# Kernel tuning notes

Hardware: AMD Instinct MI355X
Metric: run time of the kernel (lower is better)

Reference implementation:

```python
import jax, jax.numpy as jnp
import numpy as np


def setup_inputs() -> dict:
    key = jax.random.key(0)
    k1, k2 = jax.random.split(key)
    N, D, O, K = 65536, 256, 256, 8  # tokens, inputdim, outdim, degree+1
    gridsize = 8
    x = jax.random.normal(k1, (N, D), dtype=jnp.float32)
    # init stddev = 1/(sqrt(inputdim)*sqrt(gridsize)) as in the module
    std = 1.0 / (np.sqrt(D) * np.sqrt(gridsize))
    cheby_coeffs = jax.random.normal(k2, (O, D, K), dtype=jnp.float32) * std
    bias = jnp.zeros((1, O), dtype=jnp.float32)
    return {"x": x, "cheby_coeffs": cheby_coeffs, "bias": bias}


def reference(x, cheby_coeffs, bias):
    # x: (N, D); cheby_coeffs: (O, D, K); bias: (1, O)
    K = cheby_coeffs.shape[-1]
    xt = jnp.tanh(x)                       # squash into [-1, 1]
    theta = jnp.arccos(xt)                 # (N, D)
    n = jnp.arange(K, dtype=x.dtype)       # Chebyshev orders 0..degree
    # T_n(xt) = cos(n * arccos(xt)), matching the original per-degree loop
    T = jnp.cos(theta[..., None] * n)      # (N, D, K)
    y = jnp.einsum('ndk,odk->no', T, cheby_coeffs)  # (N, O)
    y = y + bias
    return y
```

## Files before the change

kernel.cpp:

```cpp
#include <hip/hip_runtime.h>
#include <hip/hip_bf16.h>

typedef __attribute__((ext_vector_type(4)))  int   i32x4;
typedef __attribute__((ext_vector_type(16))) int   i32x16;

#define DIM_D 256
#define DIM_O 256
#define DIM_K 8
#define BM 128
#define NCHUNK 16
#define NSTEP 4
#define MAGIC 12582912.f

__global__ __launch_bounds__(256) void pack_w_kernel(
    const float* __restrict__ coeffs,
    unsigned int* __restrict__ wp,
    float* __restrict__ scales)
{
    const int o = blockIdx.x;
    const int d = threadIdx.x;
    const float* cp = coeffs + ((size_t)o * DIM_D + d) * DIM_K;
    float4 c0 = *(const float4*)cp;
    float4 c1 = *(const float4*)(cp + 4);

    float m = fmaxf(fmaxf(fmaxf(fabsf(c0.x), fabsf(c0.y)),
                          fmaxf(fabsf(c0.z), fabsf(c0.w))),
                    fmaxf(fmaxf(fabsf(c1.x), fabsf(c1.y)),
                          fmaxf(fabsf(c1.z), fabsf(c1.w))));
    #pragma unroll
    for (int i = 32; i >= 1; i >>= 1)
        m = fmaxf(m, __shfl_xor(m, i));
    __shared__ float wm[4];
    if ((d & 63) == 0) wm[d >> 6] = m;
    __syncthreads();
    const float sc = fmaxf(fmaxf(fmaxf(wm[0], wm[1]), fmaxf(wm[2], wm[3])),
                           1e-30f);
    if (d == 0) scales[o] = sc;

    const float inv = 127.0f / sc;
    unsigned f0 = __float_as_uint(__builtin_fmaf(c0.x, inv, MAGIC));
    unsigned f1 = __float_as_uint(__builtin_fmaf(c0.y, inv, MAGIC));
    unsigned f2 = __float_as_uint(__builtin_fmaf(c0.z, inv, MAGIC));
    unsigned f3 = __float_as_uint(__builtin_fmaf(c0.w, inv, MAGIC));
    unsigned f4 = __float_as_uint(__builtin_fmaf(c1.x, inv, MAGIC));
    unsigned f5 = __float_as_uint(__builtin_fmaf(c1.y, inv, MAGIC));
    unsigned f6 = __float_as_uint(__builtin_fmaf(c1.z, inv, MAGIC));
    unsigned f7 = __float_as_uint(__builtin_fmaf(c1.w, inv, MAGIC));
    unsigned rA = __builtin_amdgcn_perm(f1, f0, 0x00000400u);
    unsigned rB = __builtin_amdgcn_perm(f3, f2, 0x00000400u);
    unsigned rC = __builtin_amdgcn_perm(f5, f4, 0x00000400u);
    unsigned rD = __builtin_amdgcn_perm(f7, f6, 0x00000400u);
    unsigned lo = __builtin_amdgcn_perm(rB, rA, 0x05040100u);
    unsigned hi = __builtin_amdgcn_perm(rD, rC, 0x05040100u);

    const int base = (((d >> 2) * 8 + (o >> 5)) * 64
                      + ((d >> 1) & 1) * 32 + (o & 31)) * 4 + (d & 1) * 2;
    wp[base]     = lo;
    wp[base + 1] = hi;
}

__device__ __forceinline__ void cheb_q8(float xs, unsigned int* o2) {
    float e2 = __expf(2.f * xs);
    float r  = __builtin_amdgcn_rcpf(e2 + 1.f);
    float T1 = __builtin_fmaf(-2.f, r, 1.f);
    float tx = T1 + T1;
    float T2 = __builtin_fmaf(tx, T1, -1.f);
    float T3 = __builtin_fmaf(tx, T2, -T1);
    float T4 = __builtin_fmaf(tx, T3, -T2);
    float T5 = __builtin_fmaf(tx, T4, -T3);
    float T6 = __builtin_fmaf(tx, T5, -T4);
    float T7 = __builtin_fmaf(tx, T6, -T5);
    unsigned f1 = __float_as_uint(__builtin_fmaf(T1, 127.f, MAGIC));
    unsigned f2 = __float_as_uint(__builtin_fmaf(T2, 127.f, MAGIC));
    unsigned f3 = __float_as_uint(__builtin_fmaf(T3, 127.f, MAGIC));
    unsigned f4 = __float_as_uint(__builtin_fmaf(T4, 127.f, MAGIC));
    unsigned f5 = __float_as_uint(__builtin_fmaf(T5, 127.f, MAGIC));
    unsigned f6 = __float_as_uint(__builtin_fmaf(T6, 127.f, MAGIC));
    unsigned f7 = __float_as_uint(__builtin_fmaf(T7, 127.f, MAGIC));
    unsigned rA = __builtin_amdgcn_perm(f2, f1, 0x00000400u);
    unsigned rC = __builtin_amdgcn_perm(f5, f4, 0x00000400u);
    unsigned rD = __builtin_amdgcn_perm(f7, f6, 0x00000400u);
    o2[0] = __builtin_amdgcn_perm(f3, rA, 0x0401000Cu) | 127u;
    o2[1] = __builtin_amdgcn_perm(rD, rC, 0x05040100u);
}

__global__ __launch_bounds__(256, 2) void cfkan_kernel(
    const float* __restrict__ x,
    const i32x4* __restrict__ wp8,
    const float* __restrict__ scales,
    const float* __restrict__ bias,
    float* __restrict__ y)
{
    __shared__ unsigned char Abuf[2][BM][128];

    const int t = threadIdx.x;
    const int w = t >> 6;
    const int l = t & 63;
    const int m = l & 31;
    const int h = l >> 5;
    const int bid = (int)blockIdx.x;
    const int cpx = (int)gridDim.x >> 3;
    const int row0 = ((bid & 7) * cpx + (bid >> 3)) * BM;

    i32x16 acc[4][2];
    #pragma unroll
    for (int rt = 0; rt < 4; ++rt)
        #pragma unroll
        for (int ct = 0; ct < 2; ++ct)
            #pragma unroll
            for (int qi = 0; qi < 16; ++qi)
                acc[rt][ct][qi] = 0;

    const int lrow = t >> 1;
    const int half = t & 1;
    const float* xrow = x + (size_t)(row0 + lrow) * DIM_D + half * 8;

#define READA(DST, AB, S) do {                                             \
    const int _so = (((2 * (S) + h) ^ (m & 7)) * 16);                      \
    DST[0] = *(const i32x4*)&AB[      m][_so];                             \
    DST[1] = *(const i32x4*)&AB[ 32 + m][_so];                             \
    DST[2] = *(const i32x4*)&AB[ 64 + m][_so];                             \
    DST[3] = *(const i32x4*)&AB[ 96 + m][_so];                             \
} while (0)
#define LOADB2(DST, SG) do {                                               \
    DST[0] = wp8[((SG) * 8 + w * 2 + 0) * 64 + l];                         \
    DST[1] = wp8[((SG) * 8 + w * 2 + 1) * 64 + l];                         \
} while (0)
#define STAGE2(ANX, S, X0, X1) do {                                        \
    union { unsigned int u[4]; i32x4 v; } _tv;                             \
    cheb_q8(X0, &_tv.u[0]);                                                \
    cheb_q8(X1, &_tv.u[2]);                                                \
    *(i32x4*)&ANX[lrow][(((half * 4 + (S)) ^ (lrow & 7)) * 16)] = _tv.v;   \
} while (0)
#define SOFT_BARRIER() do {                                                \
    asm volatile("s_waitcnt lgkmcnt(0)" ::: "memory");                     \
    __builtin_amdgcn_s_barrier();                                          \
    __builtin_amdgcn_sched_barrier(0);                                     \
} while (0)

    float xv[8];
    {
        float4 a0 = *(const float4*)xrow;
        float4 a1 = *(const float4*)(xrow + 4);
        float xs[8] = {a0.x, a0.y, a0.z, a0.w, a1.x, a1.y, a1.z, a1.w};
        #pragma unroll
        for (int s = 0; s < 4; ++s)
            STAGE2(Abuf[0], s, xs[2 * s], xs[2 * s + 1]);
        float4 b0 = *(const float4*)(xrow + 16);
        float4 b1 = *(const float4*)(xrow + 16 + 4);
        xv[0] = b0.x; xv[1] = b0.y; xv[2] = b0.z; xv[3] = b0.w;
        xv[4] = b1.x; xv[5] = b1.y; xv[6] = b1.z; xv[7] = b1.w;
    }
    i32x4 bq[NSTEP + 2][2];
    LOADB2(bq[0], 0);
    LOADB2(bq[1], 1);
    SOFT_BARRIER();
    i32x4 r[4], rn[4];
    READA(r, Abuf[0], 0);

    #pragma unroll 1
    for (int c = 0; c < NCHUNK; ++c) {
        const unsigned char (*A)[128] = Abuf[c & 1];
        unsigned char (*ANX)[128]     = Abuf[(c & 1) ^ 1];
        const bool stage = (c < NCHUNK - 1);
        float4 xn0, xn1;
        if (c + 2 < NCHUNK) {
            xn0 = *(const float4*)(xrow + (c + 2) * 16);
            xn1 = *(const float4*)(xrow + (c + 2) * 16 + 4);
        }

        #pragma unroll
        for (int s = 0; s < NSTEP; ++s) {
            LOADB2(bq[s + 2], (c * 4 + s + 2) & 63);
            if (s < NSTEP - 1) READA(rn, A, s + 1);

            __builtin_amdgcn_s_setprio(1);
            #pragma unroll
            for (int rt = 0; rt < 4; ++rt) {
                acc[rt][0] = __builtin_amdgcn_mfma_i32_32x32x32_i8(
                    r[rt], bq[s][0], acc[rt][0], 0, 0, 0);
                acc[rt][1] = __builtin_amdgcn_mfma_i32_32x32x32_i8(
                    r[rt], bq[s][1], acc[rt][1], 0, 0, 0);
            }
            __builtin_amdgcn_s_setprio(0);

            if (stage) STAGE2(ANX, s, xv[2 * s], xv[2 * s + 1]);

            if (s < NSTEP - 1) { r[0] = rn[0]; r[1] = rn[1]; r[2] = rn[2]; r[3] = rn[3]; }
        }
        bq[0][0] = bq[4][0]; bq[0][1] = bq[4][1];
        bq[1][0] = bq[5][0]; bq[1][1] = bq[5][1];
        if (c + 2 < NCHUNK) {
            xv[0] = xn0.x; xv[1] = xn0.y; xv[2] = xn0.z; xv[3] = xn0.w;
            xv[4] = xn1.x; xv[5] = xn1.y; xv[6] = xn1.z; xv[7] = xn1.w;
        }
        SOFT_BARRIER();
        if (c < NCHUNK - 1) READA(r, ANX, 0);
    }

    #pragma unroll
    for (int ct = 0; ct < 2; ++ct) {
        const int col = w * 64 + ct * 32 + m;
        const float sf = scales[col] * (1.f / 16129.f);
        const float bv = bias[col];
        #pragma unroll
        for (int rt = 0; rt < 4; ++rt) {
            #pragma unroll
            for (int qi = 0; qi < 16; ++qi) {
                const int grow = row0 + rt * 32 + (qi & 3) + 8 * (qi >> 2) + 4 * h;
                y[(size_t)grow * DIM_O + col] =
                    __builtin_fmaf((float)acc[rt][ct][qi], sf, bv);
            }
        }
    }
#undef READA
#undef LOADB2
#undef STAGE2
#undef SOFT_BARRIER
}

extern "C" void kernel_launch(void* const* d_in, const int* in_sizes, int n_in,
                              void* d_out, int out_size, void* d_ws, size_t ws_size,
                              hipStream_t stream) {
    const float* x      = (const float*)d_in[0];
    const float* coeffs = (const float*)d_in[1];
    const float* bias   = (const float*)d_in[2];
    float* y = (float*)d_out;
    float*        scales = (float*)d_ws;
    unsigned int* wp     = (unsigned int*)((char*)d_ws + 1024);

    const int n_tokens = in_sizes[0] / DIM_D;

    pack_w_kernel<<<DIM_O, 256, 0, stream>>>(coeffs, wp, scales);
    cfkan_kernel<<<n_tokens / BM, 256, 0, stream>>>(
        x, (const i32x4*)wp, scales, bias, y);
}
```

Measured before the change: 54.32 us.

## Double K-chunk size to halve barriers and restage A in second half

Each chunk now covers 32 input features instead of 16, so the LDS A-buffer doubles to 256 bytes per row and the main loop runs 8 iterations with 8 MFMA steps each, halving the number of block barriers. The x prefetch distance drops from two chunks to one. The Chebyshev quantize-and-store of the next chunk is moved into steps 4-7 of the current chunk. The B register ring grows to 10 entries, which raises VGPR pressure, and the shorter x prefetch distance may expose global load latency. LDS per block doubles as well, so occupancy at 2 blocks per CU may be at risk.

```diff
diff --git a/kernel.cpp b/kernel.cpp
--- a/kernel.cpp
+++ b/kernel.cpp
@@ -8,8 +8,8 @@
 #define DIM_O 256
 #define DIM_K 8
 #define BM 128
-#define NCHUNK 16
-#define NSTEP 4
+#define NCHUNK 8
+#define NSTEP 8
 #define MAGIC 12582912.f
 
 __global__ __launch_bounds__(256) void pack_w_kernel(
@@ -91,7 +91,7 @@
     const float* __restrict__ bias,
     float* __restrict__ y)
 {
-    __shared__ unsigned char Abuf[2][BM][128];
+    __shared__ unsigned char Abuf[2][BM][256];
 
     const int t = threadIdx.x;
     const int w = t >> 6;
@@ -113,7 +113,7 @@
 
     const int lrow = t >> 1;
     const int half = t & 1;
-    const float* xrow = x + (size_t)(row0 + lrow) * DIM_D + half * 8;
+    const float* xrow = x + (size_t)(row0 + lrow) * DIM_D + half * 16;
 
 #define READA(DST, AB, S) do {                                             \
     const int _so = (((2 * (S) + h) ^ (m & 7)) * 16);                      \
@@ -126,11 +126,11 @@
     DST[0] = wp8[((SG) * 8 + w * 2 + 0) * 64 + l];                         \
     DST[1] = wp8[((SG) * 8 + w * 2 + 1) * 64 + l];                         \
 } while (0)
-#define STAGE2(ANX, S, X0, X1) do {                                        \
+#define STAGE2(ANX, P, X0, X1) do {                                        \
     union { unsigned int u[4]; i32x4 v; } _tv;                             \
     cheb_q8(X0, &_tv.u[0]);                                                \
     cheb_q8(X1, &_tv.u[2]);                                                \
-    *(i32x4*)&ANX[lrow][(((half * 4 + (S)) ^ (lrow & 7)) * 16)] = _tv.v;   \
+    *(i32x4*)&ANX[lrow][(((half * 8 + (P)) ^ (lrow & 7)) * 16)] = _tv.v;   \
 } while (0)
 #define SOFT_BARRIER() do {                                                \
     asm volatile("s_waitcnt lgkmcnt(0)" ::: "memory");                     \
@@ -138,18 +138,19 @@
     __builtin_amdgcn_sched_barrier(0);                                     \
 } while (0)
 
-    float xv[8];
+    float xv[16];
     {
-        float4 a0 = *(const float4*)xrow;
+        float4 a0 = *(const float4*)(xrow);
         float4 a1 = *(const float4*)(xrow + 4);
-        float xs[8] = {a0.x, a0.y, a0.z, a0.w, a1.x, a1.y, a1.z, a1.w};
-        #pragma unroll
-        for (int s = 0; s < 4; ++s)
-            STAGE2(Abuf[0], s, xs[2 * s], xs[2 * s + 1]);
-        float4 b0 = *(const float4*)(xrow + 16);
-        float4 b1 = *(const float4*)(xrow + 16 + 4);
-        xv[0] = b0.x; xv[1] = b0.y; xv[2] = b0.z; xv[3] = b0.w;
-        xv[4] = b1.x; xv[5] = b1.y; xv[6] = b1.z; xv[7] = b1.w;
+        float4 a2 = *(const float4*)(xrow + 8);
+        float4 a3 = *(const float4*)(xrow + 12);
+        xv[0]=a0.x; xv[1]=a0.y; xv[2]=a0.z; xv[3]=a0.w;
+        xv[4]=a1.x; xv[5]=a1.y; xv[6]=a1.z; xv[7]=a1.w;
+        xv[8]=a2.x; xv[9]=a2.y; xv[10]=a2.z; xv[11]=a2.w;
+        xv[12]=a3.x; xv[13]=a3.y; xv[14]=a3.z; xv[15]=a3.w;
+        #pragma unroll
+        for (int p = 0; p < 8; ++p)
+            STAGE2(Abuf[0], p, xv[2 * p], xv[2 * p + 1]);
     }
     i32x4 bq[NSTEP + 2][2];
     LOADB2(bq[0], 0);
@@ -160,18 +161,21 @@
 
     #pragma unroll 1
     for (int c = 0; c < NCHUNK; ++c) {
-        const unsigned char (*A)[128] = Abuf[c & 1];
-        unsigned char (*ANX)[128]     = Abuf[(c & 1) ^ 1];
+        const unsigned char (*A)[256] = Abuf[c & 1];
+        unsigned char (*ANX)[256]     = Abuf[(c & 1) ^ 1];
         const bool stage = (c < NCHUNK - 1);
-        float4 xn0, xn1;
-        if (c + 2 < NCHUNK) {
-            xn0 = *(const float4*)(xrow + (c + 2) * 16);
-            xn1 = *(const float4*)(xrow + (c + 2) * 16 + 4);
+
+        float4 a0, a1, a2, a3;
+        if (stage) {
+            a0 = *(const float4*)(xrow + (c + 1) * 32);
+            a1 = *(const float4*)(xrow + (c + 1) * 32 + 4);
+            a2 = *(const float4*)(xrow + (c + 1) * 32 + 8);
+            a3 = *(const float4*)(xrow + (c + 1) * 32 + 12);
         }
 
         #pragma unroll
         for (int s = 0; s < NSTEP; ++s) {
-            LOADB2(bq[s + 2], (c * 4 + s + 2) & 63);
+            LOADB2(bq[s + 2], (c * 8 + s + 2) & 63);
             if (s < NSTEP - 1) READA(rn, A, s + 1);
 
             __builtin_amdgcn_s_setprio(1);
@@ -184,16 +188,23 @@
             }
             __builtin_amdgcn_s_setprio(0);
 
-            if (stage) STAGE2(ANX, s, xv[2 * s], xv[2 * s + 1]);
+            if (s == 3 && stage) {
+                xv[0]=a0.x; xv[1]=a0.y; xv[2]=a0.z; xv[3]=a0.w;
+                xv[4]=a1.x; xv[5]=a1.y; xv[6]=a1.z; xv[7]=a1.w;
+                xv[8]=a2.x; xv[9]=a2.y; xv[10]=a2.z; xv[11]=a2.w;
+                xv[12]=a3.x; xv[13]=a3.y; xv[14]=a3.z; xv[15]=a3.w;
+            }
+            if (s >= 4 && stage) {
+                const int p0 = (s - 4) * 2;
+                STAGE2(ANX, p0,     xv[2 * p0],     xv[2 * p0 + 1]);
+                STAGE2(ANX, p0 + 1, xv[2 * p0 + 2], xv[2 * p0 + 3]);
+            }
 
             if (s < NSTEP - 1) { r[0] = rn[0]; r[1] = rn[1]; r[2] = rn[2]; r[3] = rn[3]; }
         }
-        bq[0][0] = bq[4][0]; bq[0][1] = bq[4][1];
-        bq[1][0] = bq[5][0]; bq[1][1] = bq[5][1];
-        if (c + 2 < NCHUNK) {
-            xv[0] = xn0.x; xv[1] = xn0.y; xv[2] = xn0.z; xv[3] = xn0.w;
-            xv[4] = xn1.x; xv[5] = xn1.y; xv[6] = xn1.z; xv[7] = xn1.w;
-        }
+        bq[0][0] = bq[8][0]; bq[0][1] = bq[8][1];
+        bq[1][0] = bq[9][0]; bq[1][1] = bq[9][1];
+
         SOFT_BARRIER();
         if (c < NCHUNK - 1) READA(r, ANX, 0);
     }
```

Measured after the change: 53.85 us. No clear change (-0.9%).
